# Kernel tuning notes

Measured on AMD Instinct MI355X. Metric: run time of the kernel, lower is better.

The kernel has to match this reference:

```python
import jax, jax.numpy as jnp
import numpy as np

L0, L1, L2 = 32, 16, 8
NS, NB = 512, 256
CUT = 7.0
N, E, G = 16384, 131072, 16
FEAT = L0 + 3 * L1 + 5 * L2  # 120


def setup_inputs() -> dict:
    key = jax.random.key(0)
    ks = jax.random.split(key, 16)
    rn = lambda k, s, sc=1.0: jax.random.normal(k, s, jnp.float32) * sc
    inp = {}
    inp['nodes'] = rn(ks[0], (N, FEAT))
    inp['pos'] = rn(ks[1], (N, 3)) * 5.0
    inp['cell'] = rn(ks[2], (G, 3, 3))
    inp['edge_shift'] = rn(ks[3], (E, 3))
    # tensor-product path weights (e3nn FullyConnectedTensorProduct, uvw mode)
    inp['W0'] = rn(ks[4], (L0, L0, NS))
    inp['W1'] = rn(ks[5], (L1, L1, NS))
    inp['W2'] = rn(ks[6], (L2, L2, NS))
    inp['ln_g'] = jnp.ones((NS,), jnp.float32)
    inp['ln_b'] = jnp.zeros((NS,), jnp.float32)
    inp['df_w1'] = rn(ks[7], (NB, 1024), NB ** -0.5)
    inp['df_b1'] = jnp.zeros((1024,), jnp.float32)
    inp['df_w2'] = rn(ks[8], (1024, NS), 1024 ** -0.5)
    inp['df_b2'] = jnp.zeros((NS,), jnp.float32)
    inp['mi_w1'] = rn(ks[9], (NS, 1024), NS ** -0.5)
    inp['mi_b1'] = jnp.zeros((1024,), jnp.float32)
    inp['mi_w2'] = rn(ks[10], (1024, 1024), 1024 ** -0.5)
    inp['mi_b2'] = jnp.zeros((1024,), jnp.float32)
    inp['mo_w'] = rn(ks[11], (1024, 1), 1024 ** -0.5)
    inp['mo_b'] = jnp.zeros((1,), jnp.float32)
    inp['edge_index'] = jax.random.randint(ks[12], (2, E), 0, N)
    inp['batch_vec'] = jnp.sort(jax.random.randint(ks[13], (N,), 0, G))
    return inp


def _split_irreps(x):
    x0 = x[:, :L0]                                   # (E, L0) scalars 0e
    x1 = x[:, L0:L0 + 3 * L1].reshape(-1, L1, 3)      # (E, L1, 3) vectors 1o
    x2 = x[:, L0 + 3 * L1:].reshape(-1, L2, 5)        # (E, L2, 5) 2e
    return x0, x1, x2


def reference(nodes, pos, cell, edge_shift, W0, W1, W2, ln_g, ln_b,
              df_w1, df_b1, df_w2, df_b2, mi_w1, mi_b1, mi_w2, mi_b2,
              mo_w, mo_b, edge_index, batch_vec):
    src, dst = edge_index[0], edge_index[1]
    # periodic-image translation vector per edge
    bcell = cell[batch_vec[src]]                      # (E,3,3)
    tvec = jnp.einsum('ei,eij->ej', edge_shift, bcell)
    radvec = pos[dst] - pos[src] + tvec               # (E,3)
    dist = jnp.linalg.norm(radvec, axis=1, keepdims=True)  # (E,1)
    r = 1.0 / (dist + 1e-6)
    # Bessel radial embedding with cutoff CUT, NB basis functions
    n = jnp.arange(1, NB + 1, dtype=jnp.float32)
    emb = jnp.sqrt(2.0 / CUT) * jnp.sin(n * jnp.pi * r / CUT) / r  # (E,NB)
    distfilter = jax.nn.silu(emb @ df_w1 + df_b1) @ df_w2 + df_b2  # (E,NS)

    # symmetrized fully-connected tensor product -> 0e scalars
    # 0.5*(tp(xs,xd)+tp(xd,xs)) == contraction of euv with symmetrized W
    xs0, xs1, xs2 = _split_irreps(nodes[src])
    xd0, xd1, xd2 = _split_irreps(nodes[dst])
    fan = jnp.sqrt(jnp.float32(L0 * L0 + L1 * L1 + L2 * L2))  # element path norm
    sym = lambda W: 0.5 * (W + W.transpose(1, 0, 2))
    e0 = jnp.einsum('eu,ev->euv', xs0, xd0)
    mixed = jnp.einsum('euv,uvw->ew', e0, sym(W0)) / fan
    e1 = jnp.einsum('eui,evi->euv', xs1, xd1)
    mixed = mixed + jnp.einsum('euv,uvw->ew', e1, sym(W1)) / (fan * jnp.sqrt(3.0))
    e2 = jnp.einsum('eui,evi->euv', xs2, xd2)
    mixed = mixed + jnp.einsum('euv,uvw->ew', e2, sym(W2)) / (fan * jnp.sqrt(5.0))

    # LayerNorm over numscalars
    mu = jnp.mean(mixed, axis=-1, keepdims=True)
    var = jnp.mean((mixed - mu) ** 2, axis=-1, keepdims=True)
    mixednorm = (mixed - mu) * jax.lax.rsqrt(var + 1e-5) * ln_g + ln_b

    reg = mixednorm * distfilter
    h = jax.nn.silu(reg @ mi_w1 + mi_b1)
    h = jax.nn.silu(h @ mi_w2 + mi_b2)
    return h @ mo_w + mo_b  # (E,1)
```

## Files before the change

kernel.cpp:

```cpp
#include <hip/hip_runtime.h>

#define EE 131072
#define NNODE 16384
#define FEAT 120
#define NS 512
#define NB 256
#define KCAT 1344

typedef unsigned short u16;
typedef __bf16 bf16x8 __attribute__((ext_vector_type(8)));
typedef float f32x4 __attribute__((ext_vector_type(4)));
typedef unsigned short ushort8 __attribute__((ext_vector_type(8)));

__device__ __forceinline__ float b2f(u16 u) {
  union { unsigned int i; float f; } x; x.i = ((unsigned int)u) << 16; return x.f;
}
__device__ __forceinline__ u16 f2b(float f) {
  union { float f; unsigned int i; } x; x.f = f;
  unsigned int lsb = (x.i >> 16) & 1u;
  x.i += 0x7fffu + lsb;
  return (u16)(x.i >> 16);
}
__device__ __forceinline__ u16 f2b_fast(float f) {
  __bf16 h = (__bf16)f;
  union { __bf16 h; u16 u; } x; x.h = h; return x.u;
}
__device__ __forceinline__ float rdany(const void* p, long i, int f32) {
  return f32 ? ((const float*)p)[i] : b2f(((const u16*)p)[i]);
}

__device__ __forceinline__ void gload16(const u16* g, u16* l) {
  __builtin_amdgcn_global_load_lds(
      (__attribute__((address_space(1))) void*)(u16*)g,
      (__attribute__((address_space(3))) void*)l, 16, 0, 0);
}

struct PrepArgs {
  long cum[20];
  const void* src[19];
  u16* dst[19];
  float* outf;
  int* flag;
  const u16* nodes;
};

__global__ __launch_bounds__(256) void megaprep(PrepArgs a) {
  __shared__ int scnt[4];
  {
    u16 v = a.nodes[threadIdx.x];
    int e = (v >> 7) & 0xFF;
    unsigned long long b = __ballot(e >= 0x48);
    if ((threadIdx.x & 63) == 0) scnt[threadIdx.x >> 6] = __popcll(b);
  }
  __syncthreads();
  const int f32 = (scnt[0] + scnt[1] + scnt[2] + scnt[3]) >= 16;
  if (blockIdx.x == 0 && threadIdx.x == 0) *a.flag = f32;

  long i = (long)blockIdx.x * 256 + threadIdx.x;
  const long total = a.cum[19];
  if (i < total) {
    int s = 0;
    while (i >= a.cum[s + 1]) s++;
    long local = i - a.cum[s];
    a.dst[s][local] = f32 ? f2b(((const float*)a.src[s])[local])
                          : ((const u16*)a.src[s])[local];
  } else {
    long j = i - total;
    if (j < EE) a.outf[j] = 0.f;
  }
}

struct WprepArgs {
  const u16* tin[4];
  u16* tout[4];
  const u16 *W0, *W1, *W2;
  u16* wcT;
};

__device__ __forceinline__ void do_transpose(const u16* in, u16* out, int R, int C, int rem) {
  __shared__ u16 tile[32][33];
  const int bx = C >> 5;
  const int c0 = (rem % bx) * 32, r0 = (rem / bx) * 32;
  const int tx = threadIdx.x & 31, ty = threadIdx.x >> 5;
  for (int i = 0; i < 32; i += 8) {
    int r = r0 + ty + i, c = c0 + tx;
    if (r < R && c < C) tile[ty + i][tx] = in[(long)r * C + c];
  }
  __syncthreads();
  for (int i = 0; i < 32; i += 8) {
    int r = r0 + tx, c = c0 + ty + i;
    if (r < R && c < C) out[(long)c * R + r] = tile[tx][ty + i];
  }
}

__global__ __launch_bounds__(256) void wprep(WprepArgs a) {
  int b = blockIdx.x;
  if (b < 256) { do_transpose(a.tin[0], a.tout[0], 256, 1024, b); return; }
  b -= 256;
  if (b < 512) { do_transpose(a.tin[1], a.tout[1], 1024, 512, b); return; }
  b -= 512;
  if (b < 512) { do_transpose(a.tin[2], a.tout[2], 512, 1024, b); return; }
  b -= 512;
  if (b < 1024) { do_transpose(a.tin[3], a.tout[3], 1024, 1024, b); return; }
  b -= 1024;
  int idx = b * 256 + threadIdx.x;
  if (idx >= NS * KCAT) return;
  int w = idx / KCAT, k = idx - w * KCAT;
  const float fan = 36.66060556f;
  float val;
  if (k < 1024) {
    int u = k >> 5, v = k & 31;
    val = 0.5f * (b2f(a.W0[(u * 32 + v) * NS + w]) + b2f(a.W0[(v * 32 + u) * NS + w])) / fan;
  } else if (k < 1280) {
    int j = k - 1024;
    int u = j >> 4, v = j & 15;
    val = 0.5f * (b2f(a.W1[(u * 16 + v) * NS + w]) + b2f(a.W1[(v * 16 + u) * NS + w])) /
          (fan * 1.7320508076f);
  } else {
    int j = k - 1280;
    int u = j >> 3, v = j & 7;
    val = 0.5f * (b2f(a.W2[(u * 8 + v) * NS + w]) + b2f(a.W2[(v * 8 + u) * NS + w])) /
          (fan * 2.2360679775f);
  }
  a.wcT[idx] = f2b(val);
}

__global__ __launch_bounds__(256) void edge_prep(
    const u16* __restrict__ nodes, const void* __restrict__ pos, const void* __restrict__ cell,
    const void* __restrict__ shift, const int* __restrict__ eidx, const int* __restrict__ batch,
    u16* __restrict__ emb, u16* __restrict__ ocat, int e0, const int* __restrict__ flag) {
  const int wave = threadIdx.x >> 6, lane = threadIdx.x & 63;
  const int el = blockIdx.x * 4 + wave;
  const int e = e0 + el;
  const int f32 = *flag;
  __shared__ u16 sxs[4][FEAT], sxd[4][FEAT];
  const int src = eidx[e], dst = eidx[EE + e];
  for (int i = lane; i < FEAT; i += 64) {
    sxs[wave][i] = nodes[(long)src * FEAT + i];
    sxd[wave][i] = nodes[(long)dst * FEAT + i];
  }
  __syncthreads();
  const int b = batch[src];
  float s0 = rdany(shift, (long)e * 3, f32), s1 = rdany(shift, (long)e * 3 + 1, f32),
        s2 = rdany(shift, (long)e * 3 + 2, f32);
  float d2 = 0.f;
#pragma unroll
  for (int j = 0; j < 3; j++) {
    float tv = s0 * rdany(cell, b * 9 + j, f32) + s1 * rdany(cell, b * 9 + 3 + j, f32) +
               s2 * rdany(cell, b * 9 + 6 + j, f32);
    float rv = rdany(pos, dst * 3 + j, f32) - rdany(pos, src * 3 + j, f32) + tv;
    d2 += rv * rv;
  }
  float dist = sqrtf(d2);
  float r = 1.0f / (dist + 1e-6f);
  const float c0 = 0.5345224838f;
  const float pi7 = 0.44879895051f;
#pragma unroll
  for (int j = 0; j < 4; j++) {
    int n = lane + 64 * j;
    float val = c0 * sinf((float)(n + 1) * pi7 * r) / r;
    emb[(long)el * NB + n] = f2b(val);
  }
  const u16* xs = sxs[wave];
  const u16* xd = sxd[wave];
  u16* orow = ocat + (long)el * KCAT;
#pragma unroll
  for (int j = 0; j < 16; j++) {
    int k = lane + 64 * j;
    int u = k >> 5, v = k & 31;
    orow[k] = f2b(b2f(xs[u]) * b2f(xd[v]));
  }
#pragma unroll
  for (int j = 0; j < 4; j++) {
    int k = lane + 64 * j;
    int u = k >> 4, v = k & 15;
    float s = 0.f;
#pragma unroll
    for (int i = 0; i < 3; i++) s += b2f(xs[32 + u * 3 + i]) * b2f(xd[32 + v * 3 + i]);
    orow[1024 + k] = f2b(s);
  }
  {
    int u = lane >> 3, v = lane & 7;
    float s = 0.f;
#pragma unroll
    for (int i = 0; i < 5; i++) s += b2f(xs[80 + u * 5 + i]) * b2f(xd[80 + v * 5 + i]);
    orow[1280 + lane] = f2b(s);
  }
}

#define STGA(buf, h, part, kk)                                             \
  gload16(Ag + ((h)*128 + (part)*64) * (long)K + (kk),                      \
          &lA[buf][(h)*8192 + (part)*4096 + tid * 8])
#define STGB(buf, h, part, kk)                                             \
  gload16(Bg + ((h)*128 + (part)*64) * (long)K + (kk),                      \
          &lB[buf][(h)*8192 + (part)*4096 + tid * 8])
#define RDA(buf, fm, ks)                                                   \
  (*(const bf16x8*)((const char*)&lA[buf][0] +                             \
                    ((wm * 128 + (fm)*16 + row_l) * 128 + ((ks) ? ir1 : ir0))))
#define RDB(buf, fn, ks)                                                   \
  (*(const bf16x8*)((const char*)&lB[buf][0] +                             \
                    ((wn * 64 + (fn)*16 + row_l) * 128 + ((ks) ? ir1 : ir0))))
#define MF16(a, b, c) __builtin_amdgcn_mfma_f32_16x16x32_bf16(a, b, c, 0, 0, 0)
#define MFQ(mh, nh)                                                        \
  do {                                                                     \
    _Pragma("unroll") for (int f = 0; f < 4; f++)                          \
        _Pragma("unroll") for (int g = 0; g < 2; g++)                      \
            _Pragma("unroll") for (int ks = 0; ks < 2; ks++)               \
                acc[(mh)*4 + f][(nh)*2 + g] =                              \
        MF16(af[f][ks], bf[(nh)*2 + g][ks], acc[(mh)*4 + f][(nh)*2 + g]);  \
  } while (0)

template <int ACT, int OF32, int HEAD>
__global__ __launch_bounds__(512, 2) void gemm_bt(const u16* __restrict__ A,
                                                  const u16* __restrict__ BT,
                                                  const u16* __restrict__ bias,
                                                  void* __restrict__ Cv,
                                                  const u16* __restrict__ hw,
                                                  float* __restrict__ outf, int N, int K) {
  __shared__ __align__(16) u16 lA[2][16384];
  __shared__ __align__(16) u16 lB[2][16384];
  const int tid = threadIdx.x;
  const int lane = tid & 63;
  const int wave = tid >> 6;
  const int wm = wave >> 2, wn = wave & 3;
  const int row_l = lane & 15;
  const int kq16 = (lane >> 4) << 4;
  const int swz = (row_l & 7) << 4;
  const int ir0 = kq16 ^ swz;
  const int ir1 = (64 + kq16) ^ swz;

  const int nbn = N >> 8;
  int idx = blockIdx.x;
  if ((gridDim.x & 7) == 0) {
    int per = gridDim.x >> 3;
    idx = (blockIdx.x & 7) * per + (blockIdx.x >> 3);
  }
  const int mi = idx / nbn;
  const int ni = idx - mi * nbn;
  const long m0 = (long)mi * 256;
  const int n0 = ni << 8;
  const int nk = K >> 6;

  const int srow = tid >> 3;
  const int gseg = (tid & 7) ^ (srow & 7);
  const u16* Ag = A + (m0 + srow) * (long)K + gseg * 8;
  const u16* Bg = BT + (long)(n0 + srow) * K + gseg * 8;

  f32x4 acc[8][4];
#pragma unroll
  for (int i = 0; i < 8; i++)
#pragma unroll
    for (int j = 0; j < 4; j++)
#pragma unroll
      for (int q = 0; q < 4; q++) acc[i][j][q] = 0.f;

  STGA(0, 0, 0, 0); STGA(0, 0, 1, 0); STGA(0, 1, 0, 0); STGA(0, 1, 1, 0);
  STGB(0, 0, 0, 0); STGB(0, 0, 1, 0); STGB(0, 1, 0, 0); STGB(0, 1, 1, 0);
  if (nk > 1) {
    STGA(1, 0, 0, 64); STGA(1, 0, 1, 64); STGA(1, 1, 0, 64); STGA(1, 1, 1, 64);
    STGB(1, 0, 0, 64); STGB(1, 0, 1, 64); STGB(1, 1, 0, 64); STGB(1, 1, 1, 64);
    asm volatile("s_waitcnt vmcnt(8)" ::: "memory");
  } else {
    asm volatile("s_waitcnt vmcnt(0)" ::: "memory");
  }
  __builtin_amdgcn_s_barrier();

  bf16x8 af[4][2], bf[4][2];

  for (int t = 0; t < nk; ++t) {
    const int cur = t & 1;
    const int kN2 = (t + 2) << 6;
    const bool p2 = (t + 2) < nk;

#pragma unroll
    for (int f = 0; f < 4; f++) { af[f][0] = RDA(cur, f, 0); af[f][1] = RDA(cur, f, 1); }
#pragma unroll
    for (int g = 0; g < 2; g++) { bf[g][0] = RDB(cur, g, 0); bf[g][1] = RDB(cur, g, 1); }
    __builtin_amdgcn_s_barrier();
    asm volatile("s_waitcnt lgkmcnt(0)" ::: "memory");
    __builtin_amdgcn_s_setprio(1);
    MFQ(0, 0);
    __builtin_amdgcn_s_setprio(0);
    __builtin_amdgcn_s_barrier();

#pragma unroll
    for (int g = 0; g < 2; g++) { bf[2 + g][0] = RDB(cur, 2 + g, 0); bf[2 + g][1] = RDB(cur, 2 + g, 1); }
    __builtin_amdgcn_s_barrier();
    asm volatile("s_waitcnt lgkmcnt(0)" ::: "memory");
    __builtin_amdgcn_s_setprio(1);
    MFQ(0, 1);
    __builtin_amdgcn_s_setprio(0);
    __builtin_amdgcn_s_barrier();

#pragma unroll
    for (int f = 0; f < 4; f++) { af[f][0] = RDA(cur, 4 + f, 0); af[f][1] = RDA(cur, 4 + f, 1); }
    if (p2) { STGB(cur, 0, 0, kN2); STGB(cur, 0, 1, kN2); }
    __builtin_amdgcn_s_barrier();
    asm volatile("s_waitcnt lgkmcnt(0)" ::: "memory");
    __builtin_amdgcn_s_setprio(1);
    MFQ(1, 0);
    __builtin_amdgcn_s_setprio(0);
    __builtin_amdgcn_s_barrier();

    if (p2) {
      STGB(cur, 1, 0, kN2); STGB(cur, 1, 1, kN2);
      STGA(cur, 0, 0, kN2); STGA(cur, 0, 1, kN2);
      STGA(cur, 1, 0, kN2); STGA(cur, 1, 1, kN2);
    }
    __builtin_amdgcn_s_setprio(1);
    MFQ(1, 1);
    __builtin_amdgcn_s_setprio(0);
    if (p2)
      asm volatile("s_waitcnt vmcnt(8)" ::: "memory");
    else
      asm volatile("s_waitcnt vmcnt(0)" ::: "memory");
    __builtin_amdgcn_s_barrier();
  }

  const int rql = (lane >> 4) * 2;
  const int cl = lane & 15;
  float* Cf = (float*)Cv;
  u16* Cb = (u16*)Cv;
  if (HEAD) {
    float bv[4], hv[4];
#pragma unroll
    for (int g = 0; g < 4; g++) {
      const int col = n0 + wn * 64 + g * 16 + cl;
      bv[g] = b2f(bias[col]);
      hv[g] = b2f(hw[col]);
    }
#pragma unroll
    for (int fm = 0; fm < 8; fm++) {
#pragma unroll
      for (int q = 0; q < 4; q++) {
        float s = 0.f;
#pragma unroll
        for (int g = 0; g < 4; g++) {
          float v = acc[fm][g][q] + bv[g];
          if (ACT) v = __fdividef(v, 1.0f + __expf(-v));
          s += v * hv[g];
        }
        s += __shfl_xor(s, 1);
        s += __shfl_xor(s, 2);
        s += __shfl_xor(s, 4);
        s += __shfl_xor(s, 8);
        if (cl == 0) {
          long row = m0 + wm * 128 + fm * 16 + rql * 2 + q;
          atomicAdd(&outf[row], s);
        }
      }
    }
  } else {
#pragma unroll
    for (int fm = 0; fm < 8; fm++) {
#pragma unroll
      for (int g = 0; g < 4; g++) {
        const int col = n0 + wn * 64 + g * 16 + cl;
        const float bvv = bias ? b2f(bias[col]) : 0.0f;
#pragma unroll
        for (int q = 0; q < 4; q++) {
          long row = m0 + wm * 128 + fm * 16 + rql * 2 + q;
          float v = acc[fm][g][q] + bvv;
          if (ACT) v = __fdividef(v, 1.0f + __expf(-v));
          if (OF32)
            Cf[row * N + col] = v;
          else
            Cb[row * N + col] = f2b_fast(v);
        }
      }
    }
  }
}

__global__ __launch_bounds__(256) void ln_mul_k(const float* __restrict__ mixed,
                                                const u16* __restrict__ g,
                                                const u16* __restrict__ bvec,
                                                u16* __restrict__ dfreg) {
  const int wave = threadIdx.x >> 6, lane = threadIdx.x & 63;
  const long e = (long)blockIdx.x * 4 + wave;
  const float* row = mixed + e * NS;
  float x[8];
  f32x4 v0 = *(const f32x4*)&row[lane * 8];
  f32x4 v1 = *(const f32x4*)&row[lane * 8 + 4];
#pragma unroll
  for (int j = 0; j < 4; j++) { x[j] = v0[j]; x[4 + j] = v1[j]; }
  float s = 0.f, sq = 0.f;
#pragma unroll
  for (int j = 0; j < 8; j++) { s += x[j]; sq += x[j] * x[j]; }
  for (int o = 32; o; o >>= 1) { s += __shfl_xor(s, o); sq += __shfl_xor(sq, o); }
  float mu = s * (1.0f / 512.0f);
  float var = sq * (1.0f / 512.0f) - mu * mu;
  float rstd = rsqrtf(var + 1e-5f);
  u16* drow = dfreg + e * NS;
  ushort8 dv = *(const ushort8*)&drow[lane * 8];
  ushort8 ov;
#pragma unroll
  for (int j = 0; j < 8; j++) {
    int c = lane * 8 + j;
    float val = (x[j] - mu) * rstd * b2f(g[c]) + b2f(bvec[c]);
    ov[j] = f2b(val * b2f(dv[j]));
  }
  *(ushort8*)&drow[lane * 8] = ov;
}

__global__ __launch_bounds__(256) void head_finish(const float* __restrict__ outf,
                                                   const u16* __restrict__ b,
                                                   void* __restrict__ out,
                                                   const int* __restrict__ flag) {
  int e = blockIdx.x * 256 + threadIdx.x;
  float v = outf[e] + b2f(b[0]);
  if (*flag)
    ((float*)out)[e] = v;
  else
    ((u16*)out)[e] = f2b(v);
}

extern "C" void kernel_launch(void* const* d_in, const int* in_sizes, int n_in, void* d_out,
                              int out_size, void* d_ws, size_t ws_size, hipStream_t stream) {
  const int* eidx = (const int*)d_in[19];
  const int* batch = (const int*)d_in[20];

  char* ws = (char*)d_ws;
  size_t off = 0;
  auto alloc = [&](size_t bytes) {
    char* p = ws + off;
    off += (bytes + 255) & ~(size_t)255;
    return p;
  };

  int* flag = (int*)alloc(256);
  float* outf = (float*)alloc((size_t)EE * 4);

  PrepArgs pa;
  u16* cv[19];
  long cum = 0;
  for (int i = 0; i < 19; i++) {
    long n = in_sizes[i];
    cv[i] = (u16*)alloc((size_t)n * 2);
    pa.cum[i] = cum;
    pa.src[i] = d_in[i];
    pa.dst[i] = cv[i];
    cum += n;
  }
  pa.cum[19] = cum;
  pa.outf = outf;
  pa.flag = flag;
  pa.nodes = (const u16*)d_in[0];
  {
    long tot = cum + EE;
    megaprep<<<(int)((tot + 255) / 256), 256, 0, stream>>>(pa);
  }
  const u16* nodes = cv[0];
  const u16* ln_g = cv[7];
  const u16* ln_b = cv[8];
  const u16* df_b1 = cv[10];
  const u16* df_b2 = cv[12];
  const u16* mi_b1 = cv[14];
  const u16* mi_b2 = cv[16];
  const u16* mo_w = cv[17];
  const u16* mo_b = cv[18];

  u16* w1T = (u16*)alloc(1024 * 256 * 2);
  u16* w2T = (u16*)alloc(512 * 1024 * 2);
  u16* m1T = (u16*)alloc(1024 * 512 * 2);
  u16* m2T = (u16*)alloc((size_t)1024 * 1024 * 2);
  u16* wcT = (u16*)alloc((size_t)NS * KCAT * 2);

  WprepArgs wa;
  wa.tin[0] = cv[9];  wa.tout[0] = w1T;
  wa.tin[1] = cv[11]; wa.tout[1] = w2T;
  wa.tin[2] = cv[13]; wa.tout[2] = m1T;
  wa.tin[3] = cv[15]; wa.tout[3] = m2T;
  wa.W0 = cv[4]; wa.W1 = cv[5]; wa.W2 = cv[6];
  wa.wcT = wcT;
  wprep<<<4992, 256, 0, stream>>>(wa);

  int nchunk = 1;
  while (nchunk < 64) {
    size_t CHs = (size_t)(EE / nchunk);
    size_t need = off + CHs * 6272 + 8192;
    if (need <= ws_size) break;
    nchunk <<= 1;
  }
  const int CH = EE / nchunk;

  u16* ocat = (u16*)alloc((size_t)CH * KCAT * 2);
  u16* emb = (u16*)alloc((size_t)CH * NB * 2);
  u16* h1 = (u16*)alloc((size_t)CH * 1024 * 2);
  u16* dfb = (u16*)alloc((size_t)CH * NS * 2);
  u16* h2 = ocat;
  float* mixed = (float*)h1;

  const int RB = CH / 256;
  for (int c = 0; c < nchunk; c++) {
    const int eb = c * CH;
    edge_prep<<<CH / 4, 256, 0, stream>>>(nodes, d_in[1], d_in[2], d_in[3], eidx, batch, emb,
                                          ocat, eb, flag);

    gemm_bt<1, 0, 0><<<RB * 4, 512, 0, stream>>>(emb, w1T, df_b1, h1, nullptr, nullptr, 1024, 256);
    gemm_bt<0, 0, 0><<<RB * 2, 512, 0, stream>>>(h1, w2T, df_b2, dfb, nullptr, nullptr, 512, 1024);

    gemm_bt<0, 1, 0><<<RB * 2, 512, 0, stream>>>(ocat, wcT, nullptr, mixed, nullptr, nullptr, 512,
                                                 1344);

    ln_mul_k<<<CH / 4, 256, 0, stream>>>(mixed, ln_g, ln_b, dfb);

    gemm_bt<1, 0, 0><<<RB * 4, 512, 0, stream>>>(dfb, m1T, mi_b1, h2, nullptr, nullptr, 1024, 512);
    gemm_bt<1, 0, 1><<<RB * 4, 512, 0, stream>>>(h2, m2T, mi_b2, nullptr, mo_w, outf + eb, 1024,
                                                 1024);
  }
  head_finish<<<EE / 256, 256, 0, stream>>>(outf, mo_b, d_out, flag);
}
```

Before: 1.406 ms.

## Software-pipeline LDS fragment reads across MFMA quadrants and trim GEMM barriers

Restructures the GEMM main loop so LDS fragment reads for the next quadrant, and for the next k-tile's first A/B fragments, are issued while the current MFMA quadrant runs. It uses separate register sets (af0/af1, b01/b23) instead of waiting on lgkmcnt before each quadrant. The change drops several workgroup barriers per iteration and switches the global-load wait to vmcnt(0) before the mid-loop barrier. This aims to hide LDS latency and cut synchronization, at the cost of more VGPRs and the risk of LDS read/write hazards if the buffer reuse ordering is wrong.

Measured after the change: 1.336 ms. -4.9%, faster.

```diff
diff --git a/kernel.cpp b/kernel.cpp
--- a/kernel.cpp
+++ b/kernel.cpp
@@ -201,13 +201,13 @@
   (*(const bf16x8*)((const char*)&lB[buf][0] +                             \
                     ((wn * 64 + (fn)*16 + row_l) * 128 + ((ks) ? ir1 : ir0))))
 #define MF16(a, b, c) __builtin_amdgcn_mfma_f32_16x16x32_bf16(a, b, c, 0, 0, 0)
-#define MFQ(mh, nh)                                                        \
+#define MFQn(mh, nh, Af, Bf)                                               \
   do {                                                                     \
     _Pragma("unroll") for (int f = 0; f < 4; f++)                          \
         _Pragma("unroll") for (int g = 0; g < 2; g++)                      \
             _Pragma("unroll") for (int ks = 0; ks < 2; ks++)               \
                 acc[(mh)*4 + f][(nh)*2 + g] =                              \
-        MF16(af[f][ks], bf[(nh)*2 + g][ks], acc[(mh)*4 + f][(nh)*2 + g]);  \
+        MF16(Af[f][ks], Bf[g][ks], acc[(mh)*4 + f][(nh)*2 + g]);           \
   } while (0)
 
 template <int ACT, int OF32, int HEAD>
@@ -265,56 +265,60 @@
   }
   __builtin_amdgcn_s_barrier();
 
-  bf16x8 af[4][2], bf[4][2];
+  bf16x8 af0[4][2], af1[4][2], b01[2][2], b23[2][2];
+
+#pragma unroll
+  for (int f = 0; f < 4; f++) { af0[f][0] = RDA(0, f, 0); af0[f][1] = RDA(0, f, 1); }
+#pragma unroll
+  for (int g = 0; g < 2; g++) { b01[g][0] = RDB(0, g, 0); b01[g][1] = RDB(0, g, 1); }
 
   for (int t = 0; t < nk; ++t) {
-    const int cur = t & 1;
+    const int cur = t & 1, nxt = cur ^ 1;
     const int kN2 = (t + 2) << 6;
+    const bool p1 = (t + 1) < nk;
     const bool p2 = (t + 2) < nk;
 
 #pragma unroll
-    for (int f = 0; f < 4; f++) { af[f][0] = RDA(cur, f, 0); af[f][1] = RDA(cur, f, 1); }
-#pragma unroll
-    for (int g = 0; g < 2; g++) { bf[g][0] = RDB(cur, g, 0); bf[g][1] = RDB(cur, g, 1); }
+    for (int g = 0; g < 2; g++) { b23[g][0] = RDB(cur, 2 + g, 0); b23[g][1] = RDB(cur, 2 + g, 1); }
+    __builtin_amdgcn_sched_barrier(0);
+    __builtin_amdgcn_s_setprio(1);
+    MFQn(0, 0, af0, b01);
+    __builtin_amdgcn_s_setprio(0);
+
+#pragma unroll
+    for (int f = 0; f < 4; f++) { af1[f][0] = RDA(cur, 4 + f, 0); af1[f][1] = RDA(cur, 4 + f, 1); }
+    __builtin_amdgcn_sched_barrier(0);
+    __builtin_amdgcn_s_setprio(1);
+    MFQn(0, 1, af0, b23);
+    __builtin_amdgcn_s_setprio(0);
+
+    asm volatile("s_waitcnt vmcnt(0)" ::: "memory");
     __builtin_amdgcn_s_barrier();
-    asm volatile("s_waitcnt lgkmcnt(0)" ::: "memory");
+    if (p1) {
+#pragma unroll
+      for (int f = 0; f < 4; f++) { af0[f][0] = RDA(nxt, f, 0); af0[f][1] = RDA(nxt, f, 1); }
+    }
+    if (p2) { STGB(cur, 0, 0, kN2); STGB(cur, 0, 1, kN2); }
+    __builtin_amdgcn_sched_barrier(0);
     __builtin_amdgcn_s_setprio(1);
-    MFQ(0, 0);
+    MFQn(1, 0, af1, b01);
     __builtin_amdgcn_s_setprio(0);
+
     __builtin_amdgcn_s_barrier();
-
-#pragma unroll
-    for (int g = 0; g < 2; g++) { bf[2 + g][0] = RDB(cur, 2 + g, 0); bf[2 + g][1] = RDB(cur, 2 + g, 1); }
-    __builtin_amdgcn_s_barrier();
-    asm volatile("s_waitcnt lgkmcnt(0)" ::: "memory");
-    __builtin_amdgcn_s_setprio(1);
-    MFQ(0, 1);
-    __builtin_amdgcn_s_setprio(0);
-    __builtin_amdgcn_s_barrier();
-
-#pragma unroll
-    for (int f = 0; f < 4; f++) { af[f][0] = RDA(cur, 4 + f, 0); af[f][1] = RDA(cur, 4 + f, 1); }
-    if (p2) { STGB(cur, 0, 0, kN2); STGB(cur, 0, 1, kN2); }
-    __builtin_amdgcn_s_barrier();
-    asm volatile("s_waitcnt lgkmcnt(0)" ::: "memory");
-    __builtin_amdgcn_s_setprio(1);
-    MFQ(1, 0);
-    __builtin_amdgcn_s_setprio(0);
-    __builtin_amdgcn_s_barrier();
-
     if (p2) {
       STGB(cur, 1, 0, kN2); STGB(cur, 1, 1, kN2);
       STGA(cur, 0, 0, kN2); STGA(cur, 0, 1, kN2);
       STGA(cur, 1, 0, kN2); STGA(cur, 1, 1, kN2);
     }
+    __builtin_amdgcn_sched_barrier(0);
     __builtin_amdgcn_s_setprio(1);
-    MFQ(1, 1);
+    MFQn(1, 1, af1, b23);
     __builtin_amdgcn_s_setprio(0);
-    if (p2)
-      asm volatile("s_waitcnt vmcnt(8)" ::: "memory");
-    else
-      asm volatile("s_waitcnt vmcnt(0)" ::: "memory");
-    __builtin_amdgcn_s_barrier();
+    if (p1) {
+#pragma unroll
+      for (int g = 0; g < 2; g++) { b01[g][0] = RDB(nxt, g, 0); b01[g][1] = RDB(nxt, g, 1); }
+      __builtin_amdgcn_sched_barrier(0);
+    }
   }
 
   const int rql = (lane >> 4) * 2;
```
